# Performance work log

Hardware: AMD Instinct MI355X
Metric: run time of the kernel (lower is better)

## Reference

```python
import jax, jax.numpy as jnp
import numpy as np

N = 100000      # nodes
E = 1600000     # edges
F_IN = 128      # n_feat
AGG = 48        # agg_hidden
FC = 192        # fc_hidden
NC = 10         # n_class
ED = 4          # edge_dim
SLOPE = 0.2     # GATv2 LeakyReLU negative slope
N_LAYER = 3


def _glorot(k, shape):
    fan = shape[-1]
    return (jax.random.normal(k, shape, jnp.float32) / np.sqrt(fan)).astype(jnp.float32)


def setup_inputs() -> dict:
    key = jax.random.key(0)
    ks = jax.random.split(key, 40)
    inp = {}
    inp["x"] = jax.random.normal(ks[0], (N, F_IN), jnp.float32)
    inp["edge_index"] = jax.random.randint(ks[1], (2, E), 0, N)
    inp["edge_attr"] = jax.random.normal(ks[2], (E, ED), jnp.float32)
    dims = [F_IN, AGG, AGG]
    i = 3
    for l in range(N_LAYER):
        d = dims[l]
        inp[f"Wl{l}"] = _glorot(ks[i], (AGG, d)); i += 1   # lin_l weight
        inp[f"bl{l}"] = jnp.zeros((AGG,), jnp.float32)
        inp[f"Wr{l}"] = _glorot(ks[i], (AGG, d)); i += 1   # lin_r weight
        inp[f"br{l}"] = jnp.zeros((AGG,), jnp.float32)
        inp[f"We{l}"] = _glorot(ks[i], (AGG, ED)); i += 1  # lin_edge weight (no bias)
        inp[f"att{l}"] = _glorot(ks[i], (AGG,)); i += 1    # attention vector a
        inp[f"b{l}"] = jnp.zeros((AGG,), jnp.float32)      # output bias
    inp["fc1_w"] = _glorot(ks[i], (FC, AGG)); i += 1
    inp["fc1_b"] = jnp.zeros((FC,), jnp.float32)
    inp["fc2_w"] = _glorot(ks[i], (NC, FC)); i += 1
    inp["fc2_b"] = jnp.zeros((NC,), jnp.float32)
    return inp


def _gatv2(x, src, dst, ea, Wl, bl, Wr, br, We, att, b):
    # GATv2Conv, heads=1, concat=True, eval mode (dropout off)
    xl = x @ Wl.T + bl                                   # [N, AGG] source transform
    xr = x @ Wr.T + br                                   # [N, AGG] target transform
    m = jax.nn.leaky_relu(xl[src] + xr[dst] + ea @ We.T, SLOPE)  # [E, AGG]
    e = m @ att                                          # [E] attention logits
    # segment softmax over incoming edges of each destination node
    emax = jax.ops.segment_max(e, dst, num_segments=N)
    ee = jnp.exp(e - emax[dst])
    den = jax.ops.segment_sum(ee, dst, num_segments=N)
    alpha = ee / jnp.maximum(den, 1e-16)[dst]            # [E]
    out = jax.ops.segment_sum(alpha[:, None] * xl[src], dst, num_segments=N)
    return out + b


def reference(x, edge_index, edge_attr,
              Wl0, bl0, Wr0, br0, We0, att0, b0,
              Wl1, bl1, Wr1, br1, We1, att1, b1,
              Wl2, bl2, Wr2, br2, We2, att2, b2,
              fc1_w, fc1_b, fc2_w, fc2_b):
    src, dst = edge_index[0], edge_index[1]
    layers = [
        (Wl0, bl0, Wr0, br0, We0, att0, b0),
        (Wl1, bl1, Wr1, br1, We1, att1, b1),
        (Wl2, bl2, Wr2, br2, We2, att2, b2),
    ]
    h = x
    for p in layers:
        h = jax.nn.relu(_gatv2(h, src, dst, edge_attr, *p))
    g = jnp.sum(h, axis=0)                               # readout='sum' -> [AGG]
    g = jax.nn.relu(g @ fc1_w.T + fc1_b)                 # [FC]
    return jax.nn.softmax(g @ fc2_w.T + fc2_b)           # [NC]
```

## Files before the change

kernel.cpp:

```cpp
#include <hip/hip_runtime.h>
#include <hip/hip_fp16.h>
#include <math.h>

#define NNODE 100000
#define NEDGE 1600000
#define FIN   128
#define AGG   48
#define FCH   192
#define NCLS  10
#define SLOPE 0.2f
#define L2E   1.44269504088896340736f

#define NBUCK 391
#define BCAP  4992
#define EPB   2048

__device__ __forceinline__ float2 h2f(int p) {
    union { int i; __half2 h; } u; u.i = p;
    return __half22float2(u.h);
}
__device__ __forceinline__ int f2h(float a, float b) {
    union { __half2 h; int i; } u;
    u.h = __floats2half2_rn(a, b);
    return u.i;
}


__global__ __launch_bounds__(256) void binA_kernel(const int* __restrict__ ei,
                                                   const float4* __restrict__ ea,
                                                   int* __restrict__ deg,
                                                   int* __restrict__ bcnt,
                                                   int4* __restrict__ bbuf) {
    __shared__ int  hist[NBUCK];
    __shared__ int  lofs[NBUCK];
    __shared__ int  gbase[NBUCK];
    __shared__ int  scA[512], scB[512];
    __shared__ int  gidx[EPB];
    __shared__ int4 stage[EPB];

    const int t = threadIdx.x;
    const int wgbase = blockIdx.x * EPB;
    const int nvalid = min(EPB, NEDGE - wgbase);

    for (int i = t; i < NBUCK; i += 256) hist[i] = 0;
    __syncthreads();

    int d[8], rank[8];
#pragma unroll
    for (int i = 0; i < 8; ++i) {
        int e = wgbase + i * 256 + t;
        if (e < NEDGE) {
            d[i] = ei[NEDGE + e];
            rank[i] = atomicAdd(&hist[d[i] >> 8], 1);
            atomicAdd(&deg[d[i]], 1);
        } else d[i] = -1;
    }
    __syncthreads();

    {
        scA[t] = (t < NBUCK) ? hist[t] : 0;
        scA[t + 256] = (t + 256 < NBUCK) ? hist[t + 256] : 0;
        __syncthreads();
        int* src = scA; int* dst = scB;
#pragma unroll
        for (int o = 1; o < 512; o <<= 1) {
            int i0 = t, i1 = t + 256;
            int v0 = src[i0] + ((i0 >= o) ? src[i0 - o] : 0);
            int v1 = src[i1] + ((i1 >= o) ? src[i1 - o] : 0);
            __syncthreads();
            dst[i0] = v0; dst[i1] = v1;
            __syncthreads();
            int* tmp = src; src = dst; dst = tmp;
        }
        if (t < NBUCK) lofs[t] = src[t] - hist[t];
        if (t + 256 < NBUCK) lofs[t + 256] = src[t + 256] - hist[t + 256];
    }
    for (int i = t; i < NBUCK; i += 256)
        gbase[i] = hist[i] ? atomicAdd(&bcnt[i], hist[i]) : 0;
    __syncthreads();

#pragma unroll
    for (int i = 0; i < 8; ++i) {
        int e = wgbase + i * 256 + t;
        if (e < NEDGE) {
            int b = d[i] >> 8;
            int slot = lofs[b] + rank[i];
            int gp = gbase[b] + rank[i];
            float4 v = ea[e];
            stage[slot] = make_int4(ei[e], d[i], f2h(v.x, v.y), f2h(v.z, v.w));
            gidx[slot] = (gp < BCAP) ? (b * BCAP + gp) : -1;
        }
    }
    __syncthreads();

    for (int i = t; i < nvalid; i += 256) {
        int gi = gidx[i];
        if (gi >= 0) bbuf[gi] = stage[i];
    }
}

__global__ void scan1_kernel(const int* __restrict__ deg, int* __restrict__ starts,
                             int* __restrict__ bsum) {
    __shared__ int s[256];
    int t = threadIdx.x;
    int i = blockIdx.x * 256 + t;
    int v = (i < NNODE) ? deg[i] : 0;
    s[t] = v;
    __syncthreads();
    int acc = v;
    for (int o = 1; o < 256; o <<= 1) {
        int x = (t >= o) ? s[t - o] : 0;
        __syncthreads();
        acc += x;
        s[t] = acc;
        __syncthreads();
    }
    if (i < NNODE) starts[i] = acc - v;
    if (t == 255) bsum[blockIdx.x] = acc;
}

__global__ void scan2_kernel(int* __restrict__ bsum, int nb) {
    __shared__ int s[512];
    int t = threadIdx.x;
    int v = (t < nb) ? bsum[t] : 0;
    s[t] = v;
    __syncthreads();
    int acc = v;
    for (int o = 1; o < 512; o <<= 1) {
        int x = (t >= o) ? s[t - o] : 0;
        __syncthreads();
        acc += x;
        s[t] = acc;
        __syncthreads();
    }
    if (t < nb) bsum[t] = acc - v;
}

__global__ void scan3_kernel(int* __restrict__ starts, const int* __restrict__ bsum) {
    int i = blockIdx.x * 256 + threadIdx.x;
    if (i < NNODE) starts[i] += bsum[blockIdx.x];
    if (i == 0) starts[NNODE] = NEDGE;
}

__global__ __launch_bounds__(1024) void binB_kernel(const int* __restrict__ bcnt,
                                                    const int4* __restrict__ bbuf,
                                                    const int* __restrict__ starts,
                                                    int4* __restrict__ edges) {
    __shared__ int lcur[256];
    const int b = blockIdx.x;
    const int t = threadIdx.x;
    if (t < 256) {
        int node = (b << 8) + t;
        lcur[t] = (node < NNODE) ? starts[node] : 0;
    }
    __syncthreads();
    int cnt = bcnt[b];
    if (cnt > BCAP) cnt = BCAP;
    for (int i = t; i < cnt; i += 1024) {
        int4 rec = bbuf[(size_t)b * BCAP + i];
        int pos = atomicAdd(&lcur[rec.y & 255], 1);
        edges[pos] = make_int4(rec.x, rec.z, rec.w, 0);
    }
}


template <int K>
__global__ __launch_bounds__(192) void transform_tiled(
    const float* __restrict__ h,
    const float* __restrict__ Wl, const float* __restrict__ bl,
    const float* __restrict__ Wr, const float* __restrict__ br,
    __half* __restrict__ xlh, float* __restrict__ xr)
{
    constexpr int NT = 48;
    constexpr int KP = K + 1;
    __shared__ float sWl[K * 48];
    __shared__ float sWr[K * 48];
    __shared__ float sH[NT * KP];

    const int t = threadIdx.x;
    const int base = blockIdx.x * NT;

    for (int idx = t; idx < 48 * K; idx += 192) {
        int k = idx / K;
        int j = idx - k * K;
        sWl[j * 48 + k] = Wl[idx];
        sWr[j * 48 + k] = Wr[idx];
    }
    for (int p = t; p < NT * (K / 4); p += 192) {
        int row = p / (K / 4);
        int c4  = p - row * (K / 4);
        int gn  = base + row;
        float4 v = (gn < NNODE) ? ((const float4*)h)[(size_t)gn * (K / 4) + c4]
                                : make_float4(0.f, 0.f, 0.f, 0.f);
        float* d = &sH[row * KP + c4 * 4];
        d[0] = v.x; d[1] = v.y; d[2] = v.z; d[3] = v.w;
    }
    __syncthreads();

    const int q  = t % 12;
    const int ng = t / 12;
    float al[3][4] = {};
    float ar[3][4] = {};

    const float4* sWl4 = (const float4*)sWl;
    const float4* sWr4 = (const float4*)sWr;
#pragma unroll 4
    for (int j = 0; j < K; ++j) {
        float4 wl4 = sWl4[j * 12 + q];
        float4 wr4 = sWr4[j * 12 + q];
        float h0 = sH[(ng + 0)  * KP + j];
        float h1 = sH[(ng + 16) * KP + j];
        float h2 = sH[(ng + 32) * KP + j];
        al[0][0] += h0 * wl4.x; al[0][1] += h0 * wl4.y; al[0][2] += h0 * wl4.z; al[0][3] += h0 * wl4.w;
        ar[0][0] += h0 * wr4.x; ar[0][1] += h0 * wr4.y; ar[0][2] += h0 * wr4.z; ar[0][3] += h0 * wr4.w;
        al[1][0] += h1 * wl4.x; al[1][1] += h1 * wl4.y; al[1][2] += h1 * wl4.z; al[1][3] += h1 * wl4.w;
        ar[1][0] += h1 * wr4.x; ar[1][1] += h1 * wr4.y; ar[1][2] += h1 * wr4.z; ar[1][3] += h1 * wr4.w;
        al[2][0] += h2 * wl4.x; al[2][1] += h2 * wl4.y; al[2][2] += h2 * wl4.z; al[2][3] += h2 * wl4.w;
        ar[2][0] += h2 * wr4.x; ar[2][1] += h2 * wr4.y; ar[2][2] += h2 * wr4.z; ar[2][3] += h2 * wr4.w;
    }

    float4 bl4 = ((const float4*)bl)[q];
    float4 br4 = ((const float4*)br)[q];
#pragma unroll
    for (int i = 0; i < 3; ++i) {
        int gn = base + ng + 16 * i;
        if (gn < NNODE) {
            int2 pk = make_int2(f2h(al[i][0] + bl4.x, al[i][1] + bl4.y),
                                f2h(al[i][2] + bl4.z, al[i][3] + bl4.w));
            ((int2*)xlh)[(size_t)gn * 16 + q] = pk;
            float4 orr = make_float4(ar[i][0] + br4.x, ar[i][1] + br4.y,
                                     ar[i][2] + br4.z, ar[i][3] + br4.w);
            ((float4*)xr)[(size_t)gn * 12 + q] = orr;
        }
    }
}

__device__ __forceinline__ float group_sum16(float v) {
#define DPP_ADD(ctrl)                                                          \
    v += __int_as_float(__builtin_amdgcn_update_dpp(                           \
        0, __float_as_int(v), ctrl, 0xf, 0xf, true))
    DPP_ADD(0xB1);
    DPP_ADD(0x4E);
    DPP_ADD(0x141);
    DPP_ADD(0x140);
#undef DPP_ADD
    return v;
}

__global__ void aggregate_kernel(const __half* __restrict__ xlh, const float* __restrict__ xr,
                                 const int* __restrict__ starts, const int4* __restrict__ edges,
                                 const float* __restrict__ We, const float* __restrict__ att,
                                 const float* __restrict__ bias,
                                 float* __restrict__ hout) {
    int node = (blockIdx.x * blockDim.x + threadIdx.x) >> 6;
    if (node >= NNODE) return;
    const int lane = threadIdx.x & 63;
    const int g = lane >> 4;
    const int r = lane & 15;
    const bool act = r < 12;
    const int rc = act ? r : 0;

    const float4* We4 = (const float4*)We;
    float4 w0 = We4[4 * rc + 0], w1 = We4[4 * rc + 1],
           w2 = We4[4 * rc + 2], w3 = We4[4 * rc + 3];
    float4 a4 = ((const float4*)att)[rc];
    float aA = act ? a4.x * L2E : 0.f;
    float aB = act ? a4.y * L2E : 0.f;
    float aC = act ? a4.z * L2E : 0.f;
    float aD = act ? a4.w * L2E : 0.f;
    float4 xr4 = ((const float4*)xr)[(size_t)node * 12 + rc];

    int s = starts[node];
    int e_end = starts[node + 1];
    float den = 0.f, ac0 = 0.f, ac1 = 0.f, ac2 = 0.f, ac3 = 0.f;

    for (int j = s; j < e_end; j += 8) {
        int j0 = j + g, j1 = j + 4 + g;
        bool v0 = j0 < e_end, v1 = j1 < e_end;
        int4 edA = edges[v0 ? j0 : j];
        int4 edB = edges[v1 ? j1 : j];
        int2 xiA = ((const int2*)xlh)[(size_t)edA.x * 16 + rc];
        int2 xiB = ((const int2*)xlh)[(size_t)edB.x * 16 + rc];

        float2 eA01 = h2f(edA.y), eA23 = h2f(edA.z);
        float2 eB01 = h2f(edB.y), eB23 = h2f(edB.z);
        float2 xA01 = h2f(xiA.x), xA23 = h2f(xiA.y);
        float2 xB01 = h2f(xiB.x), xB23 = h2f(xiB.y);

        float vA0 = fmaf(w0.w, eA23.y, fmaf(w0.z, eA23.x, fmaf(w0.y, eA01.y, fmaf(w0.x, eA01.x, xA01.x + xr4.x))));
        float vA1 = fmaf(w1.w, eA23.y, fmaf(w1.z, eA23.x, fmaf(w1.y, eA01.y, fmaf(w1.x, eA01.x, xA01.y + xr4.y))));
        float vA2 = fmaf(w2.w, eA23.y, fmaf(w2.z, eA23.x, fmaf(w2.y, eA01.y, fmaf(w2.x, eA01.x, xA23.x + xr4.z))));
        float vA3 = fmaf(w3.w, eA23.y, fmaf(w3.z, eA23.x, fmaf(w3.y, eA01.y, fmaf(w3.x, eA01.x, xA23.y + xr4.w))));
        float vB0 = fmaf(w0.w, eB23.y, fmaf(w0.z, eB23.x, fmaf(w0.y, eB01.y, fmaf(w0.x, eB01.x, xB01.x + xr4.x))));
        float vB1 = fmaf(w1.w, eB23.y, fmaf(w1.z, eB23.x, fmaf(w1.y, eB01.y, fmaf(w1.x, eB01.x, xB01.y + xr4.y))));
        float vB2 = fmaf(w2.w, eB23.y, fmaf(w2.z, eB23.x, fmaf(w2.y, eB01.y, fmaf(w2.x, eB01.x, xB23.x + xr4.z))));
        float vB3 = fmaf(w3.w, eB23.y, fmaf(w3.z, eB23.x, fmaf(w3.y, eB01.y, fmaf(w3.x, eB01.x, xB23.y + xr4.w))));

        float tA, tB;
        tA =           aA * fmaf(SLOPE, fminf(vA0, 0.f), fmaxf(vA0, 0.f));
        tA = fmaf(aB, fmaf(SLOPE, fminf(vA1, 0.f), fmaxf(vA1, 0.f)), tA);
        tA = fmaf(aC, fmaf(SLOPE, fminf(vA2, 0.f), fmaxf(vA2, 0.f)), tA);
        tA = fmaf(aD, fmaf(SLOPE, fminf(vA3, 0.f), fmaxf(vA3, 0.f)), tA);
        tB =           aA * fmaf(SLOPE, fminf(vB0, 0.f), fmaxf(vB0, 0.f));
        tB = fmaf(aB, fmaf(SLOPE, fminf(vB1, 0.f), fmaxf(vB1, 0.f)), tB);
        tB = fmaf(aC, fmaf(SLOPE, fminf(vB2, 0.f), fmaxf(vB2, 0.f)), tB);
        tB = fmaf(aD, fmaf(SLOPE, fminf(vB3, 0.f), fmaxf(vB3, 0.f)), tB);

        tA = group_sum16(tA);
        tB = group_sum16(tB);

        float pA = v0 ? exp2f(tA) : 0.f;
        float pB = v1 ? exp2f(tB) : 0.f;
        den += pA + pB;
        ac0 = fmaf(pB, xB01.x, fmaf(pA, xA01.x, ac0));
        ac1 = fmaf(pB, xB01.y, fmaf(pA, xA01.y, ac1));
        ac2 = fmaf(pB, xB23.x, fmaf(pA, xA23.x, ac2));
        ac3 = fmaf(pB, xB23.y, fmaf(pA, xA23.y, ac3));
    }

    den += __int_as_float(__builtin_amdgcn_ds_swizzle(__float_as_int(den), 0x401F));
    ac0 += __int_as_float(__builtin_amdgcn_ds_swizzle(__float_as_int(ac0), 0x401F));
    ac1 += __int_as_float(__builtin_amdgcn_ds_swizzle(__float_as_int(ac1), 0x401F));
    ac2 += __int_as_float(__builtin_amdgcn_ds_swizzle(__float_as_int(ac2), 0x401F));
    ac3 += __int_as_float(__builtin_amdgcn_ds_swizzle(__float_as_int(ac3), 0x401F));
    den += __shfl_xor(den, 32);
    ac0 += __shfl_xor(ac0, 32);
    ac1 += __shfl_xor(ac1, 32);
    ac2 += __shfl_xor(ac2, 32);
    ac3 += __shfl_xor(ac3, 32);

    if (lane < 16 && act) {
        float inv = 1.f / fmaxf(den, 1e-16f);
        float4 b4 = ((const float4*)bias)[r];
        float4 o = make_float4(fmaxf(fmaf(ac0, inv, b4.x), 0.f),
                               fmaxf(fmaf(ac1, inv, b4.y), 0.f),
                               fmaxf(fmaf(ac2, inv, b4.z), 0.f),
                               fmaxf(fmaf(ac3, inv, b4.w), 0.f));
        ((float4*)hout)[(size_t)node * 12 + r] = o;
    }
}


__global__ void readout_kernel(const float* __restrict__ h, float* __restrict__ g) {
    int wid = (blockIdx.x * blockDim.x + threadIdx.x) >> 6;
    int lane = threadIdx.x & 63;
    int nw = (gridDim.x * blockDim.x) >> 6;
    if (lane < AGG) {
        float acc = 0.f;
        for (int n = wid; n < NNODE; n += nw) acc += h[n * AGG + lane];
        atomicAdd(&g[lane], acc);
    }
}

__global__ void head_kernel(const float* __restrict__ g,
                            const float* __restrict__ fc1w, const float* __restrict__ fc1b,
                            const float* __restrict__ fc2w, const float* __restrict__ fc2b,
                            float* __restrict__ out) {
    __shared__ float sg[AGG];
    __shared__ float s1[FCH];
    __shared__ float s2[NCLS];
    int t = threadIdx.x;
    if (t < AGG) sg[t] = g[t];
    __syncthreads();
    if (t < FCH) {
        float a = fc1b[t];
        for (int j = 0; j < AGG; ++j) a += fc1w[t * AGG + j] * sg[j];
        s1[t] = fmaxf(a, 0.f);
    }
    __syncthreads();
    if (t < NCLS) {
        float a = fc2b[t];
        for (int j = 0; j < FCH; ++j) a += fc2w[t * FCH + j] * s1[j];
        s2[t] = a;
    }
    __syncthreads();
    if (t == 0) {
        float mx = s2[0];
        for (int i = 1; i < NCLS; ++i) mx = fmaxf(mx, s2[i]);
        float ex[NCLS];
        float den = 0.f;
        for (int i = 0; i < NCLS; ++i) { ex[i] = __expf(s2[i] - mx); den += ex[i]; }
        for (int i = 0; i < NCLS; ++i) out[i] = ex[i] / den;
    }
}


extern "C" void kernel_launch(void* const* d_in, const int* in_sizes, int n_in,
                              void* d_out, int out_size, void* d_ws, size_t ws_size,
                              hipStream_t stream) {
    const float* x  = (const float*)d_in[0];
    const int*   ei = (const int*)d_in[1];
    const float* ea = (const float*)d_in[2];
    const float* Wl[3], *bl[3], *Wr[3], *br[3], *We[3], *att[3], *bb[3];
    for (int l = 0; l < 3; ++l) {
        int base = 3 + l * 7;
        Wl[l]  = (const float*)d_in[base + 0];
        bl[l]  = (const float*)d_in[base + 1];
        Wr[l]  = (const float*)d_in[base + 2];
        br[l]  = (const float*)d_in[base + 3];
        We[l]  = (const float*)d_in[base + 4];
        att[l] = (const float*)d_in[base + 5];
        bb[l]  = (const float*)d_in[base + 6];
    }
    const float* fc1w = (const float*)d_in[24];
    const float* fc1b = (const float*)d_in[25];
    const float* fc2w = (const float*)d_in[26];
    const float* fc2b = (const float*)d_in[27];
    float* outp = (float*)d_out;

    char* ws = (char*)d_ws;
    __half* xlh   = (__half*)ws;
    float*  xr    = (float*)(ws + (size_t)NNODE * 64 * 2);
    int4*   bbuf  = (int4*)ws;
    size_t off = (size_t)NNODE * 64 * 2 + (size_t)NNODE * AGG * 4;
    auto take = [&](size_t bytes) -> void* {
        void* p = ws + off;
        off = (off + bytes + 255) & ~(size_t)255;
        return p;
    };
    float*  h      = (float*)take((size_t)NNODE * AGG * 4);
    int*    deg    = (int*)take((size_t)NNODE * 4);
    int*    starts = (int*)take((size_t)(NNODE + 1) * 4);
    int*    bsum   = (int*)take(1024 * 4);
    int*    bcnt   = (int*)take(NBUCK * 4);
    int4*   edges  = (int4*)take((size_t)NEDGE * 16);
    float*  g      = (float*)take(64 * 4);

    const int NB1 = (NNODE + 255) / 256;

    hipMemsetAsync(deg, 0, (size_t)NNODE * 4, stream);
    hipMemsetAsync(bcnt, 0, NBUCK * 4, stream);
    binA_kernel<<<(NEDGE + EPB - 1) / EPB, 256, 0, stream>>>(ei, (const float4*)ea,
                                                             deg, bcnt, bbuf);
    scan1_kernel<<<NB1, 256, 0, stream>>>(deg, starts, bsum);
    scan2_kernel<<<1, 512, 0, stream>>>(bsum, NB1);
    scan3_kernel<<<NB1, 256, 0, stream>>>(starts, bsum);
    binB_kernel<<<NBUCK, 1024, 0, stream>>>(bcnt, bbuf, starts, edges);

    const int TGRID = (NNODE + 47) / 48;
    const int AGRID = (NNODE + 3) / 4;

    transform_tiled<FIN><<<TGRID, 192, 0, stream>>>(x, Wl[0], bl[0], Wr[0], br[0], xlh, xr);
    aggregate_kernel<<<AGRID, 256, 0, stream>>>(xlh, xr, starts, edges,
                                                We[0], att[0], bb[0], h);
    transform_tiled<AGG><<<TGRID, 192, 0, stream>>>(h, Wl[1], bl[1], Wr[1], br[1], xlh, xr);
    aggregate_kernel<<<AGRID, 256, 0, stream>>>(xlh, xr, starts, edges,
                                                We[1], att[1], bb[1], h);
    transform_tiled<AGG><<<TGRID, 192, 0, stream>>>(h, Wl[2], bl[2], Wr[2], br[2], xlh, xr);
    aggregate_kernel<<<AGRID, 256, 0, stream>>>(xlh, xr, starts, edges,
                                                We[2], att[2], bb[2], h);

    hipMemsetAsync(g, 0, 64 * 4, stream);
    readout_kernel<<<256, 256, 0, stream>>>(h, g);
    head_kernel<<<1, 192, 0, stream>>>(g, fc1w, fc1b, fc2w, fc2b, outp);
}
```

Baseline: 510.0 us.

## Derive per-node CSR offsets inside bucket pass instead of global degree atomics

Removes the 1.6M global per-node degree atomics from the binning pass and the three-kernel node-level scan. Bucket counts are now scanned in a single small kernel, and each binB block builds a per-node histogram of its own bucket in shared memory, scans it, and writes the node start offsets. This cuts global atomic traffic and several launches. In exchange binB reads each bucket's records twice. It assumes no bucket overflows BCAP, which the earlier code also relied on.

```diff
diff --git a/kernel.cpp b/kernel.cpp
--- a/kernel.cpp
+++ b/kernel.cpp
@@ -28,7 +28,6 @@
 
 __global__ __launch_bounds__(256) void binA_kernel(const int* __restrict__ ei,
                                                    const float4* __restrict__ ea,
-                                                   int* __restrict__ deg,
                                                    int* __restrict__ bcnt,
                                                    int4* __restrict__ bbuf) {
     __shared__ int  hist[NBUCK];
@@ -52,7 +51,6 @@
         if (e < NEDGE) {
             d[i] = ei[NEDGE + e];
             rank[i] = atomicAdd(&hist[d[i] >> 8], 1);
-            atomicAdd(&deg[d[i]], 1);
         } else d[i] = -1;
     }
     __syncthreads();
@@ -99,30 +97,11 @@
     }
 }
 
-__global__ void scan1_kernel(const int* __restrict__ deg, int* __restrict__ starts,
-                             int* __restrict__ bsum) {
-    __shared__ int s[256];
-    int t = threadIdx.x;
-    int i = blockIdx.x * 256 + t;
-    int v = (i < NNODE) ? deg[i] : 0;
-    s[t] = v;
-    __syncthreads();
-    int acc = v;
-    for (int o = 1; o < 256; o <<= 1) {
-        int x = (t >= o) ? s[t - o] : 0;
-        __syncthreads();
-        acc += x;
-        s[t] = acc;
-        __syncthreads();
-    }
-    if (i < NNODE) starts[i] = acc - v;
-    if (t == 255) bsum[blockIdx.x] = acc;
-}
-
-__global__ void scan2_kernel(int* __restrict__ bsum, int nb) {
+__global__ void bscan_kernel(const int* __restrict__ bcnt, int* __restrict__ bstart,
+                             int* __restrict__ starts) {
     __shared__ int s[512];
     int t = threadIdx.x;
-    int v = (t < nb) ? bsum[t] : 0;
+    int v = (t < NBUCK) ? bcnt[t] : 0;
     s[t] = v;
     __syncthreads();
     int acc = v;
@@ -133,29 +112,45 @@
         s[t] = acc;
         __syncthreads();
     }
-    if (t < nb) bsum[t] = acc - v;
-}
-
-__global__ void scan3_kernel(int* __restrict__ starts, const int* __restrict__ bsum) {
-    int i = blockIdx.x * 256 + threadIdx.x;
-    if (i < NNODE) starts[i] += bsum[blockIdx.x];
-    if (i == 0) starts[NNODE] = NEDGE;
+    if (t < NBUCK) bstart[t] = acc - v;
+    if (t == 0) starts[NNODE] = NEDGE;
 }
 
 __global__ __launch_bounds__(1024) void binB_kernel(const int* __restrict__ bcnt,
+                                                    const int* __restrict__ bstart,
                                                     const int4* __restrict__ bbuf,
-                                                    const int* __restrict__ starts,
+                                                    int* __restrict__ starts,
                                                     int4* __restrict__ edges) {
+    __shared__ int ncnt[256];
+    __shared__ int sc[256];
     __shared__ int lcur[256];
     const int b = blockIdx.x;
     const int t = threadIdx.x;
+    if (t < 256) ncnt[t] = 0;
+    __syncthreads();
+    int cnt = min(bcnt[b], BCAP);
+    int base = bstart[b];
+    for (int i = t; i < cnt; i += 1024)
+        atomicAdd(&ncnt[bbuf[(size_t)b * BCAP + i].y & 255], 1);
+    __syncthreads();
+    int v = 0, acc = 0;
+    if (t < 256) { v = ncnt[t]; sc[t] = v; }
+    __syncthreads();
+    acc = v;
+    for (int o = 1; o < 256; o <<= 1) {
+        int x = 0;
+        if (t < 256 && t >= o) x = sc[t - o];
+        __syncthreads();
+        if (t < 256) { acc += x; sc[t] = acc; }
+        __syncthreads();
+    }
     if (t < 256) {
         int node = (b << 8) + t;
-        lcur[t] = (node < NNODE) ? starts[node] : 0;
-    }
-    __syncthreads();
-    int cnt = bcnt[b];
-    if (cnt > BCAP) cnt = BCAP;
+        int st = base + acc - v;
+        lcur[t] = st;
+        if (node < NNODE) starts[node] = st;
+    }
+    __syncthreads();
     for (int i = t; i < cnt; i += 1024) {
         int4 rec = bbuf[(size_t)b * BCAP + i];
         int pos = atomicAdd(&lcur[rec.y & 255], 1);
@@ -419,23 +414,17 @@
         return p;
     };
     float*  h      = (float*)take((size_t)NNODE * AGG * 4);
-    int*    deg    = (int*)take((size_t)NNODE * 4);
     int*    starts = (int*)take((size_t)(NNODE + 1) * 4);
-    int*    bsum   = (int*)take(1024 * 4);
     int*    bcnt   = (int*)take(NBUCK * 4);
+    int*    bstart = (int*)take((NBUCK + 1) * 4);
     int4*   edges  = (int4*)take((size_t)NEDGE * 16);
     float*  g      = (float*)take(64 * 4);
 
-    const int NB1 = (NNODE + 255) / 256;
-
-    hipMemsetAsync(deg, 0, (size_t)NNODE * 4, stream);
     hipMemsetAsync(bcnt, 0, NBUCK * 4, stream);
     binA_kernel<<<(NEDGE + EPB - 1) / EPB, 256, 0, stream>>>(ei, (const float4*)ea,
-                                                             deg, bcnt, bbuf);
-    scan1_kernel<<<NB1, 256, 0, stream>>>(deg, starts, bsum);
-    scan2_kernel<<<1, 512, 0, stream>>>(bsum, NB1);
-    scan3_kernel<<<NB1, 256, 0, stream>>>(starts, bsum);
-    binB_kernel<<<NBUCK, 1024, 0, stream>>>(bcnt, bbuf, starts, edges);
+                                                             bcnt, bbuf);
+    bscan_kernel<<<1, 512, 0, stream>>>(bcnt, bstart, starts);
+    binB_kernel<<<NBUCK, 1024, 0, stream>>>(bcnt, bstart, bbuf, starts, edges);
 
     const int TGRID = (NNODE + 47) / 48;
     const int AGRID = (NNODE + 3) / 4;
```

Result: faster. 450.6 us (-11.7%).
